# Kernel tuning notes

Hardware: AMD Instinct MI355X
Metric: run time of the kernel (lower is better)

## Reference

```python
import jax, jax.numpy as jnp
import numpy as np

N_NODES = 100000   # number of graph nodes
N_EDGES = 1000000  # number of edges
D_IN = 64          # input feature dim
D_OUT = 64         # output feature dim
N_RELS = 16        # number of relation types


def setup_inputs() -> dict:
    key = jax.random.key(0)
    k1, k2, k3, k4, k5 = jax.random.split(key, 5)
    feat = jax.random.normal(k1, (N_NODES, D_IN), dtype=jnp.float32)
    weight = jax.random.normal(k2, (N_RELS, D_IN, D_OUT), dtype=jnp.float32) * 0.05
    src = jax.random.randint(k3, (N_EDGES,), 0, N_NODES)
    dst = jax.random.randint(k4, (N_EDGES,), 0, N_NODES)
    etypes = jax.random.randint(k5, (N_EDGES,), 0, N_RELS)
    return {"feat": feat, "weight": weight, "src": src, "dst": dst, "etypes": etypes}


def reference(feat, weight, src, dst, etypes):
    # gather source-node features per edge: h = edges.src['h']
    h = feat[src]                                # [E, d_in]
    n_rels = weight.shape[0]
    e, d_out = h.shape[0], weight.shape[2]

    # gather_mm(h, weight, idx_b=etypes): m_e = h_e @ weight[etypes_e]
    # grouped-GEMM realized as R masked dense GEMMs (R is small, fixed);
    # avoids materializing the [E, d_in, d_out] gathered weight tensor.
    def step(m, rw):
        r, w_r = rw
        mask = jnp.where(etypes == r, 1.0, 0.0).astype(h.dtype)  # [E]
        m = m + mask[:, None] * (h @ w_r)                        # [E, d_out]
        return m, None

    m0 = jnp.zeros((e, d_out), dtype=h.dtype)
    m, _ = jax.lax.scan(step, m0, (jnp.arange(n_rels), weight))

    # update_all(..., fn.sum('m', 'h')): scatter-sum messages to dst nodes
    out = jax.ops.segment_sum(m, dst, num_segments=feat.shape[0])  # [N, d_out]
    return out
```

## Files before the change

kernel.cpp:

```cpp
#include <hip/hip_runtime.h>
#include <hip/hip_bf16.h>
#include <stdint.h>

#define NNODES 100000
#define NEDGES 1000000
#define NRELS 16
#define EPB 2048
#define NB ((NEDGES + EPB - 1) / EPB)
#define PADCAP (NEDGES + NRELS * 64)
#define MAXTILES (PADCAP / 64)
#define NDN NNODES
#define BKT 256
#define NBKT ((NDN + BKT - 1) / BKT)

#define FEAT_BLKS 6250
#define W_BLKS 256
#define SETUP_BLKS (FEAT_BLKS + W_BLKS + NB)
#define SCANS_BLKS (1 + (NBKT + 15) / 16)

#define OFF_FEATB    0ull
#define OFF_WT       12800000ull
#define OFF_HIST16   12931072ull
#define OFF_BBASE16  12963840ull
#define OFF_PVE      12996608ull
#define OFF_HIST391  12996864ull
#define OFF_BBASE391 13764864ull
#define OFF_BSTART   14532864ull
#define OFF_DNSTART  14534912ull
#define OFF_KEYP     14935552ull
#define OFF_INV      18935552ull
#define OFF_SRCS     22939648ull
#define OFF_MSGE     26943744ull
#define WS_NEED 155074816ull

using short8  = __attribute__((ext_vector_type(8))) short;
using floatx4 = __attribute__((ext_vector_type(4))) float;
using uintx4  = __attribute__((ext_vector_type(4))) unsigned int;

__device__ __forceinline__ unsigned short f2bf(float f) {
    union { float f; uint32_t u; } v; v.f = f;
    uint32_t u = v.u;
    return (unsigned short)((u + 0x7FFFu + ((u >> 16) & 1u)) >> 16);
}
__device__ __forceinline__ float bf2f(uint32_t u16) {
    union { uint32_t u; float f; } v; v.u = u16 << 16;
    return v.f;
}
__device__ __forceinline__ uint32_t pk2(float a, float b) {
    __hip_bfloat162 h = __float22bfloat162_rn(make_float2(a, b));
    union { __hip_bfloat162 h; uint32_t u; } v; v.h = h;
    return v.u;
}

__global__ void k_setup(const float* __restrict__ feat, const float* __restrict__ W,
                        const int* __restrict__ et, const int* __restrict__ dst,
                        unsigned short* __restrict__ featB, unsigned short* __restrict__ Wt,
                        int* __restrict__ hist16, int* __restrict__ hist391) {
    __shared__ int cnt16[16];
    __shared__ int cnt391[NBKT];
    const int b = blockIdx.x;
    if (b < FEAT_BLKS) {
        int i = (b * 256 + threadIdx.x) * 4;
        const float4 f = *(const float4*)(feat + i);
        ushort4 o;
        o.x = f2bf(f.x); o.y = f2bf(f.y); o.z = f2bf(f.z); o.w = f2bf(f.w);
        *(ushort4*)(featB + i) = o;
    } else if (b < FEAT_BLKS + W_BLKS) {
        int t = (b - FEAT_BLKS) * 256 + threadIdx.x;
        int r = t >> 12, n = (t >> 6) & 63, k = t & 63;
        Wt[t] = f2bf(W[(r << 12) + (k << 6) + n]);
    } else {
        const int bb = b - (FEAT_BLKS + W_BLKS);
        if (threadIdx.x < 16) cnt16[threadIdx.x] = 0;
        for (int t = threadIdx.x; t < NBKT; t += 256) cnt391[t] = 0;
        __syncthreads();
        int start = bb * EPB;
        int end = min(NEDGES, start + EPB);
        for (int i = start + threadIdx.x; i < end; i += 256) {
            atomicAdd(&cnt16[et[i]], 1);
            atomicAdd(&cnt391[dst[i] >> 8], 1);
        }
        __syncthreads();
        if (threadIdx.x < 16) hist16[bb * 16 + threadIdx.x] = cnt16[threadIdx.x];
        for (int t = threadIdx.x; t < NBKT; t += 256)
            hist391[bb * NBKT + t] = cnt391[t];
    }
}

__global__ void __launch_bounds__(1024)
k_scans(const int* __restrict__ hist16, int* __restrict__ bbase16,
        int* __restrict__ Pve,
        const int* __restrict__ hist391, int* __restrict__ bbase391,
        int* __restrict__ bstart) {
    int w = threadIdx.x >> 6;
    int lane = threadIdx.x & 63;
    if (blockIdx.x == 0) {
        __shared__ int s_cnt[16];
        __shared__ int s_P[17];
        int carry = 0;
        for (int c = 0; c < NB; c += 64) {
            int idx = c + lane;
            int v = (idx < NB) ? hist16[idx * 16 + w] : 0;
            int x = v;
            #pragma unroll
            for (int off = 1; off < 64; off <<= 1) {
                int y = __shfl_up(x, off);
                if (lane >= off) x += y;
            }
            if (idx < NB) bbase16[idx * 16 + w] = carry + x - v;
            carry += __shfl(x, 63);
        }
        if (lane == 0) s_cnt[w] = carry;
        __syncthreads();
        if (threadIdx.x == 0) {
            int p = 0;
            for (int r = 0; r < 16; ++r) {
                s_P[r] = p;
                Pve[r] = p;
                Pve[17 + r] = p + s_cnt[r];
                p += (s_cnt[r] + 63) & ~63;
            }
            s_P[16] = p;
            Pve[16] = p;
        }
        __syncthreads();
        int pw = s_P[w];
        for (int idx = lane; idx < NB; idx += 64)
            bbase16[idx * 16 + w] += pw;
    } else {
        int b = (blockIdx.x - 1) * 16 + w;
        if (b >= NBKT) return;
        int carry = 0;
        for (int c = 0; c < NB; c += 64) {
            int idx = c + lane;
            int v = (idx < NB) ? hist391[idx * NBKT + b] : 0;
            int x = v;
            #pragma unroll
            for (int off = 1; off < 64; off <<= 1) {
                int y = __shfl_up(x, off);
                if (lane >= off) x += y;
            }
            if (idx < NB) bbase391[idx * NBKT + b] = carry + x - v;
            carry += __shfl(x, 63);
        }
        if (lane == 0) bstart[b] = carry;
    }
}

__global__ void k_bscanB(int* __restrict__ bstart) {
    __shared__ int wtot[8];
    int t = threadIdx.x;
    int v = (t < NBKT) ? bstart[t] : 0;
    int lane = t & 63, w = t >> 6;
    int x = v;
    #pragma unroll
    for (int off = 1; off < 64; off <<= 1) {
        int y = __shfl_up(x, off);
        if (lane >= off) x += y;
    }
    if (lane == 63) wtot[w] = x;
    __syncthreads();
    int woff = 0;
    for (int i = 0; i < w; ++i) woff += wtot[i];
    if (t < NBKT) bstart[t] = woff + x - v;
    if (t == 511) {
        int total = 0;
        for (int i = 0; i < 8; ++i) total += wtot[i];
        bstart[NBKT] = total;
    }
}

__global__ void k_scatter(const int* __restrict__ et, const int* __restrict__ src,
                          const int* __restrict__ dst, const int* __restrict__ bbase16,
                          const int* __restrict__ bbase391, const int* __restrict__ bstart,
                          int* __restrict__ srcS, int* __restrict__ keyP) {
    __shared__ int base16[16];
    __shared__ int base391[NBKT];
    if (threadIdx.x < 16) base16[threadIdx.x] = bbase16[blockIdx.x * 16 + threadIdx.x];
    for (int t = threadIdx.x; t < NBKT; t += 256)
        base391[t] = bbase391[blockIdx.x * NBKT + t] + bstart[t];
    __syncthreads();
    int start = blockIdx.x * EPB;
    int end = min(NEDGES, start + EPB);
    for (int i = start + threadIdx.x; i < end; i += 256) {
        int r = et[i];
        int pos = atomicAdd(&base16[r], 1);
        srcS[pos] = src[i];
        int d = dst[i];
        int bp = atomicAdd(&base391[d >> 8], 1);
        keyP[bp] = (pos << 8) | (d & 255);
    }
}

__global__ void __launch_bounds__(256)
k_bsort(const int* __restrict__ keyP, const int* __restrict__ bstart,
        int* __restrict__ inv, int* __restrict__ dnstart) {
    __shared__ int cnt[256];
    __shared__ int nodebase[256];
    __shared__ int wtot[4];
    const int b = blockIdx.x;
    const int start = bstart[b], end = bstart[b + 1];
    const int t = threadIdx.x;
    cnt[t] = 0;
    __syncthreads();
    for (int e = start + t; e < end; e += 256)
        atomicAdd(&cnt[keyP[e] & 255], 1);
    __syncthreads();
    int v = cnt[t];
    int lane = t & 63, w = t >> 6;
    int x = v;
    #pragma unroll
    for (int off = 1; off < 64; off <<= 1) {
        int y = __shfl_up(x, off);
        if (lane >= off) x += y;
    }
    if (lane == 63) wtot[w] = x;
    __syncthreads();
    int woff = 0;
    for (int i = 0; i < w; ++i) woff += wtot[i];
    nodebase[t] = woff + x - v;
    cnt[t] = 0;
    __syncthreads();
    dnstart[b * 256 + t] = start + nodebase[t];
    if (b == NBKT - 1 && t == 255) dnstart[NBKT * 256] = end;
    for (int e = start + t; e < end; e += 256) {
        int k = keyP[e];
        int node = k & 255;
        int rk = atomicAdd(&cnt[node], 1);
        inv[k >> 8] = start + nodebase[node] + rk;
    }
}

__global__ void __launch_bounds__(256)
k_computeA(const unsigned short* __restrict__ featB,
           const unsigned short* __restrict__ Wt,
           const int* __restrict__ srcS, const int* __restrict__ Pve,
           const int* __restrict__ inv,
           unsigned short* __restrict__ msgE) {
    __shared__ float lds[4][16 * 68];
    const int w = threadIdx.x >> 6;
    const int t = blockIdx.x * 4 + w;
    const int base = t * 64;
    const int total = Pve[16];
    if (base >= total) return;
    int r = 0;
    while (base >= Pve[r + 1]) ++r;
    const int validEnd = Pve[17 + r];
    const int lane = threadIdx.x & 63;
    const int quad = lane >> 4;
    const int l16 = lane & 15;
    const int rr = lane >> 2, seg = lane & 3;

    int s[4];
    #pragma unroll
    for (int tm = 0; tm < 4; ++tm) {
        int row = base + tm * 16 + l16;
        s[tm] = (row < validEnd) ? srcS[row] : 0;
    }
    int dpos[4]; bool vld[4];
    #pragma unroll
    for (int tm = 0; tm < 4; ++tm) {
        int g = base + tm * 16 + rr;
        vld[tm] = (g < validEnd);
        dpos[tm] = vld[tm] ? inv[g] : 0;
    }
    const unsigned short* wr = Wt + (r << 12);
    short8 bfr[4][2];
    #pragma unroll
    for (int tn = 0; tn < 4; ++tn)
        #pragma unroll
        for (int ks = 0; ks < 2; ++ks)
            bfr[tn][ks] = *(const short8*)(wr + ((tn * 16 + l16) << 6) + ks * 32 + quad * 8);
    short8 a[4][2];
    #pragma unroll
    for (int tm = 0; tm < 4; ++tm) {
        const unsigned short* fp = featB + ((size_t)s[tm] << 6) + quad * 8;
        a[tm][0] = *(const short8*)(fp);
        a[tm][1] = *(const short8*)(fp + 32);
    }
    #pragma unroll
    for (int tm = 0; tm < 4; ++tm) {
        #pragma unroll
        for (int tn = 0; tn < 4; ++tn) {
            floatx4 c = {0.f, 0.f, 0.f, 0.f};
            c = __builtin_amdgcn_mfma_f32_16x16x32_bf16(a[tm][0], bfr[tn][0], c, 0, 0, 0);
            c = __builtin_amdgcn_mfma_f32_16x16x32_bf16(a[tm][1], bfr[tn][1], c, 0, 0, 0);
            #pragma unroll
            for (int j = 0; j < 4; ++j)
                lds[w][(quad * 4 + j) * 68 + tn * 16 + l16] = c[j];
        }
        if (vld[tm]) {
            const float* lp = &lds[w][rr * 68 + seg * 16];
            uintx4 o0, o1;
            o0.x = pk2(lp[0],  lp[1]);  o0.y = pk2(lp[2],  lp[3]);
            o0.z = pk2(lp[4],  lp[5]);  o0.w = pk2(lp[6],  lp[7]);
            o1.x = pk2(lp[8],  lp[9]);  o1.y = pk2(lp[10], lp[11]);
            o1.z = pk2(lp[12], lp[13]); o1.w = pk2(lp[14], lp[15]);
            uintx4* op = (uintx4*)(msgE + (size_t)dpos[tm] * 64 + seg * 16);
            op[0] = o0;
            op[1] = o1;
        }
    }
}

__global__ void __launch_bounds__(256)
k_reduce(const unsigned short* __restrict__ msgE,
         const int* __restrict__ dnstart, float* __restrict__ out) {
    int n = blockIdx.x * 4 + (threadIdx.x >> 6);
    if (n >= NDN) return;
    int lane = threadIdx.x & 63;
    int start = dnstart[n];
    int end = dnstart[n + 1];
    int c8 = (lane & 7) * 8;
    float a0 = 0.f, a1 = 0.f, a2 = 0.f, a3 = 0.f;
    float a4 = 0.f, a5 = 0.f, a6 = 0.f, a7 = 0.f;
    int row = start + (lane >> 3);
    for (; row + 8 < end; row += 16) {
        uintx4 v0 = *(const uintx4*)(msgE + (size_t)row * 64 + c8);
        uintx4 v1 = *(const uintx4*)(msgE + (size_t)(row + 8) * 64 + c8);
        a0 += bf2f(v0.x & 0xffffu); a1 += bf2f(v0.x >> 16);
        a2 += bf2f(v0.y & 0xffffu); a3 += bf2f(v0.y >> 16);
        a4 += bf2f(v0.z & 0xffffu); a5 += bf2f(v0.z >> 16);
        a6 += bf2f(v0.w & 0xffffu); a7 += bf2f(v0.w >> 16);
        a0 += bf2f(v1.x & 0xffffu); a1 += bf2f(v1.x >> 16);
        a2 += bf2f(v1.y & 0xffffu); a3 += bf2f(v1.y >> 16);
        a4 += bf2f(v1.z & 0xffffu); a5 += bf2f(v1.z >> 16);
        a6 += bf2f(v1.w & 0xffffu); a7 += bf2f(v1.w >> 16);
    }
    if (row < end) {
        uintx4 v = *(const uintx4*)(msgE + (size_t)row * 64 + c8);
        a0 += bf2f(v.x & 0xffffu); a1 += bf2f(v.x >> 16);
        a2 += bf2f(v.y & 0xffffu); a3 += bf2f(v.y >> 16);
        a4 += bf2f(v.z & 0xffffu); a5 += bf2f(v.z >> 16);
        a6 += bf2f(v.w & 0xffffu); a7 += bf2f(v.w >> 16);
    }
    #pragma unroll
    for (int m = 8; m <= 32; m <<= 1) {
        a0 += __shfl_xor(a0, m); a1 += __shfl_xor(a1, m);
        a2 += __shfl_xor(a2, m); a3 += __shfl_xor(a3, m);
        a4 += __shfl_xor(a4, m); a5 += __shfl_xor(a5, m);
        a6 += __shfl_xor(a6, m); a7 += __shfl_xor(a7, m);
    }
    if (lane < 8) {
        float* op = out + (size_t)n * 64 + lane * 8;
        *(float4*)(op)     = make_float4(a0, a1, a2, a3);
        *(float4*)(op + 4) = make_float4(a4, a5, a6, a7);
    }
}

__global__ void __launch_bounds__(256)
k_fb(const float* __restrict__ feat, const float* __restrict__ W,
     const int* __restrict__ src, const int* __restrict__ dst,
     const int* __restrict__ et, float* __restrict__ out) {
    int e = blockIdx.x * 4 + (threadIdx.x >> 6);
    if (e >= NEDGES) return;
    int c = threadIdx.x & 63;
    int s = src[e], d = dst[e], r = et[e];
    const float* fr = feat + (size_t)s * 64;
    const float* wr = W + ((size_t)r << 12);
    float acc = 0.f;
    for (int k = 0; k < 64; ++k) acc += fr[k] * wr[k * 64 + c];
    atomicAdd(out + (size_t)d * 64 + c, acc);
}

extern "C" void kernel_launch(void* const* d_in, const int* in_sizes, int n_in,
                              void* d_out, int out_size, void* d_ws, size_t ws_size,
                              hipStream_t stream) {
    const float* feat = (const float*)d_in[0];
    const float* W    = (const float*)d_in[1];
    const int* src    = (const int*)d_in[2];
    const int* dst    = (const int*)d_in[3];
    const int* et     = (const int*)d_in[4];
    float* out = (float*)d_out;
    char* ws = (char*)d_ws;

    unsigned short* featB = (unsigned short*)(ws + OFF_FEATB);
    unsigned short* Wt    = (unsigned short*)(ws + OFF_WT);
    int* hist16   = (int*)(ws + OFF_HIST16);
    int* bbase16  = (int*)(ws + OFF_BBASE16);
    int* Pve      = (int*)(ws + OFF_PVE);
    int* hist391  = (int*)(ws + OFF_HIST391);
    int* bbase391 = (int*)(ws + OFF_BBASE391);
    int* bstart   = (int*)(ws + OFF_BSTART);
    int* dnstart  = (int*)(ws + OFF_DNSTART);
    int* keyP     = (int*)(ws + OFF_KEYP);
    int* inv      = (int*)(ws + OFF_INV);
    int* srcS     = (int*)(ws + OFF_SRCS);
    unsigned short* msgE = (unsigned short*)(ws + OFF_MSGE);

    if (ws_size >= WS_NEED) {
        k_setup<<<SETUP_BLKS, 256, 0, stream>>>(feat, W, et, dst, featB, Wt,
                                                hist16, hist391);
        k_scans<<<SCANS_BLKS, 1024, 0, stream>>>(hist16, bbase16, Pve, hist391,
                                                 bbase391, bstart);
        k_bscanB<<<1, 512, 0, stream>>>(bstart);
        k_scatter<<<NB, 256, 0, stream>>>(et, src, dst, bbase16, bbase391, bstart,
                                          srcS, keyP);
        k_bsort<<<NBKT, 256, 0, stream>>>(keyP, bstart, inv, dnstart);
        k_computeA<<<(MAXTILES + 3) / 4, 256, 0, stream>>>(featB, Wt, srcS, Pve,
                                                           inv, msgE);
        k_reduce<<<(NDN + 3) / 4, 256, 0, stream>>>(msgE, dnstart, out);
    } else {
        hipMemsetAsync(d_out, 0, (size_t)out_size * sizeof(float), stream);
        k_fb<<<(NEDGES + 3) / 4, 256, 0, stream>>>(feat, W, src, dst, et, out);
    }
}
```

Before: 226.5 us.

## Sort edges by relation and source-node block to improve gather locality

The edge sort key changes from relation type alone to relation type plus a 512-node source block. Edges within each relation are then ordered by source locality, so feature gathers in the GEMM kernel hit cache more often. The cost is a much larger per-block histogram (3136 bins), a serial column scan, and a new finalize kernel. The message write-back in the compute kernel is also reshaped so each lane stores 8 bf16 values instead of 16.

```diff
diff --git a/kernel.cpp b/kernel.cpp
--- a/kernel.cpp
+++ b/kernel.cpp
@@ -10,28 +10,33 @@
 #define PADCAP (NEDGES + NRELS * 64)
 #define MAXTILES (PADCAP / 64)
 #define NDN NNODES
-#define BKT 256
-#define NBKT ((NDN + BKT - 1) / BKT)
+#define NBKT ((NDN + 255) / 256)
+#define NSB  ((NNODES + 511) / 512)
+#define NSBKT (NRELS * NSB)
 
 #define FEAT_BLKS 6250
 #define W_BLKS 256
 #define SETUP_BLKS (FEAT_BLKS + W_BLKS + NB)
-#define SCANS_BLKS (1 + (NBKT + 15) / 16)
-
-#define OFF_FEATB    0ull
-#define OFF_WT       12800000ull
-#define OFF_HIST16   12931072ull
-#define OFF_BBASE16  12963840ull
-#define OFF_PVE      12996608ull
-#define OFF_HIST391  12996864ull
-#define OFF_BBASE391 13764864ull
-#define OFF_BSTART   14532864ull
-#define OFF_DNSTART  14534912ull
-#define OFF_KEYP     14935552ull
-#define OFF_INV      18935552ull
-#define OFF_SRCS     22939648ull
-#define OFF_MSGE     26943744ull
-#define WS_NEED 155074816ull
+#define DST_SCAN_BLKS ((NBKT + 15) / 16)
+#define SRC_SCAN_BLKS ((NSBKT + 1023) / 1024)
+#define SCANS_BLKS (DST_SCAN_BLKS + SRC_SCAN_BLKS)
+
+#define OFF_FEATB     0ull
+#define OFF_WT        12800000ull
+#define OFF_COLSUM    12931072ull
+#define OFF_BKB       12943616ull
+#define OFF_PVE       12956160ull
+#define OFF_HIST391   12956416ull
+#define OFF_BBASE391  13721344ull
+#define OFF_BSTART    14486272ull
+#define OFF_DNSTART   14488064ull
+#define OFF_KEYP      14888704ull
+#define OFF_INV       18888704ull
+#define OFF_SRCS      22892800ull
+#define OFF_MSGE      26896896ull
+#define OFF_HIST3136  26896896ull
+#define OFF_BBASE3136 33030912ull
+#define WS_NEED 155027968ull
 
 using short8  = __attribute__((ext_vector_type(8))) short;
 using floatx4 = __attribute__((ext_vector_type(4))) float;
@@ -53,10 +58,11 @@
 }
 
 __global__ void k_setup(const float* __restrict__ feat, const float* __restrict__ W,
-                        const int* __restrict__ et, const int* __restrict__ dst,
+                        const int* __restrict__ et, const int* __restrict__ src,
+                        const int* __restrict__ dst,
                         unsigned short* __restrict__ featB, unsigned short* __restrict__ Wt,
-                        int* __restrict__ hist16, int* __restrict__ hist391) {
-    __shared__ int cnt16[16];
+                        int* __restrict__ hist3136, int* __restrict__ hist391) {
+    __shared__ int cnt3136[NSBKT];
     __shared__ int cnt391[NBKT];
     const int b = blockIdx.x;
     if (b < FEAT_BLKS) {
@@ -71,64 +77,32 @@
         Wt[t] = f2bf(W[(r << 12) + (k << 6) + n]);
     } else {
         const int bb = b - (FEAT_BLKS + W_BLKS);
-        if (threadIdx.x < 16) cnt16[threadIdx.x] = 0;
+        for (int t = threadIdx.x; t < NSBKT; t += 256) cnt3136[t] = 0;
         for (int t = threadIdx.x; t < NBKT; t += 256) cnt391[t] = 0;
         __syncthreads();
         int start = bb * EPB;
         int end = min(NEDGES, start + EPB);
         for (int i = start + threadIdx.x; i < end; i += 256) {
-            atomicAdd(&cnt16[et[i]], 1);
+            atomicAdd(&cnt3136[et[i] * NSB + (src[i] >> 9)], 1);
             atomicAdd(&cnt391[dst[i] >> 8], 1);
         }
         __syncthreads();
-        if (threadIdx.x < 16) hist16[bb * 16 + threadIdx.x] = cnt16[threadIdx.x];
+        for (int t = threadIdx.x; t < NSBKT; t += 256)
+            hist3136[bb * NSBKT + t] = cnt3136[t];
         for (int t = threadIdx.x; t < NBKT; t += 256)
             hist391[bb * NBKT + t] = cnt391[t];
     }
 }
 
 __global__ void __launch_bounds__(1024)
-k_scans(const int* __restrict__ hist16, int* __restrict__ bbase16,
-        int* __restrict__ Pve,
-        const int* __restrict__ hist391, int* __restrict__ bbase391,
-        int* __restrict__ bstart) {
-    int w = threadIdx.x >> 6;
-    int lane = threadIdx.x & 63;
-    if (blockIdx.x == 0) {
-        __shared__ int s_cnt[16];
-        __shared__ int s_P[17];
-        int carry = 0;
-        for (int c = 0; c < NB; c += 64) {
-            int idx = c + lane;
-            int v = (idx < NB) ? hist16[idx * 16 + w] : 0;
-            int x = v;
-            #pragma unroll
-            for (int off = 1; off < 64; off <<= 1) {
-                int y = __shfl_up(x, off);
-                if (lane >= off) x += y;
-            }
-            if (idx < NB) bbase16[idx * 16 + w] = carry + x - v;
-            carry += __shfl(x, 63);
-        }
-        if (lane == 0) s_cnt[w] = carry;
-        __syncthreads();
-        if (threadIdx.x == 0) {
-            int p = 0;
-            for (int r = 0; r < 16; ++r) {
-                s_P[r] = p;
-                Pve[r] = p;
-                Pve[17 + r] = p + s_cnt[r];
-                p += (s_cnt[r] + 63) & ~63;
-            }
-            s_P[16] = p;
-            Pve[16] = p;
-        }
-        __syncthreads();
-        int pw = s_P[w];
-        for (int idx = lane; idx < NB; idx += 64)
-            bbase16[idx * 16 + w] += pw;
-    } else {
-        int b = (blockIdx.x - 1) * 16 + w;
+k_scans(const int* __restrict__ hist391, int* __restrict__ bbase391,
+        int* __restrict__ bstart,
+        const int* __restrict__ hist3136, int* __restrict__ bbase3136,
+        int* __restrict__ colsum) {
+    if (blockIdx.x < DST_SCAN_BLKS) {
+        int w = threadIdx.x >> 6;
+        int lane = threadIdx.x & 63;
+        int b = blockIdx.x * 16 + w;
         if (b >= NBKT) return;
         int carry = 0;
         for (int c = 0; c < NB; c += 64) {
@@ -144,48 +118,101 @@
             carry += __shfl(x, 63);
         }
         if (lane == 0) bstart[b] = carry;
-    }
-}
-
-__global__ void k_bscanB(int* __restrict__ bstart) {
-    __shared__ int wtot[8];
-    int t = threadIdx.x;
-    int v = (t < NBKT) ? bstart[t] : 0;
-    int lane = t & 63, w = t >> 6;
-    int x = v;
-    #pragma unroll
-    for (int off = 1; off < 64; off <<= 1) {
-        int y = __shfl_up(x, off);
-        if (lane >= off) x += y;
-    }
-    if (lane == 63) wtot[w] = x;
-    __syncthreads();
-    int woff = 0;
-    for (int i = 0; i < w; ++i) woff += wtot[i];
-    if (t < NBKT) bstart[t] = woff + x - v;
-    if (t == 511) {
-        int total = 0;
-        for (int i = 0; i < 8; ++i) total += wtot[i];
-        bstart[NBKT] = total;
+    } else {
+        int col = (blockIdx.x - DST_SCAN_BLKS) * 1024 + threadIdx.x;
+        if (col >= NSBKT) return;
+        int carry = 0;
+        #pragma unroll 4
+        for (int i = 0; i < NB; ++i) {
+            int v = hist3136[i * NSBKT + col];
+            bbase3136[i * NSBKT + col] = carry;
+            carry += v;
+        }
+        colsum[col] = carry;
+    }
+}
+
+__global__ void __launch_bounds__(1024)
+k_finalize(int* __restrict__ bstart, const int* __restrict__ colsum,
+           int* __restrict__ bucketbase, int* __restrict__ Pve) {
+    if (blockIdx.x == 0) {
+        __shared__ int wtot[16];
+        int t = threadIdx.x;
+        int v = (t < NBKT) ? bstart[t] : 0;
+        int lane = t & 63, w = t >> 6;
+        int x = v;
+        #pragma unroll
+        for (int off = 1; off < 64; off <<= 1) {
+            int y = __shfl_up(x, off);
+            if (lane >= off) x += y;
+        }
+        if (lane == 63) wtot[w] = x;
+        __syncthreads();
+        int woff = 0;
+        for (int i = 0; i < w; ++i) woff += wtot[i];
+        if (t < NBKT) bstart[t] = woff + x - v;
+        if (t == 1023) {
+            int total = 0;
+            for (int i = 0; i < 16; ++i) total += wtot[i];
+            bstart[NBKT] = total;
+        }
+    } else {
+        __shared__ int sbb[NRELS][NSB];
+        __shared__ int s_cnt[16];
+        __shared__ int s_P[16];
+        int lane = threadIdx.x & 63, r = threadIdx.x >> 6;
+        int carry = 0;
+        for (int c = 0; c < NSB; c += 64) {
+            int idx = c + lane;
+            int v = (idx < NSB) ? colsum[r * NSB + idx] : 0;
+            int x = v;
+            #pragma unroll
+            for (int off = 1; off < 64; off <<= 1) {
+                int y = __shfl_up(x, off);
+                if (lane >= off) x += y;
+            }
+            if (idx < NSB) sbb[r][idx] = carry + x - v;
+            carry += __shfl(x, 63);
+        }
+        if (lane == 0) s_cnt[r] = carry;
+        __syncthreads();
+        if (threadIdx.x == 0) {
+            int p = 0;
+            for (int q = 0; q < 16; ++q) {
+                s_P[q] = p;
+                Pve[q] = p;
+                Pve[17 + q] = p + s_cnt[q];
+                p += (s_cnt[q] + 63) & ~63;
+            }
+            Pve[16] = p;
+        }
+        __syncthreads();
+        int pr = s_P[r];
+        for (int idx = lane; idx < NSB; idx += 64)
+            bucketbase[r * NSB + idx] = sbb[r][idx] + pr;
     }
 }
 
 __global__ void k_scatter(const int* __restrict__ et, const int* __restrict__ src,
-                          const int* __restrict__ dst, const int* __restrict__ bbase16,
+                          const int* __restrict__ dst,
+                          const int* __restrict__ bbase3136,
+                          const int* __restrict__ bucketbase,
                           const int* __restrict__ bbase391, const int* __restrict__ bstart,
                           int* __restrict__ srcS, int* __restrict__ keyP) {
-    __shared__ int base16[16];
+    __shared__ int base3136[NSBKT];
     __shared__ int base391[NBKT];
-    if (threadIdx.x < 16) base16[threadIdx.x] = bbase16[blockIdx.x * 16 + threadIdx.x];
+    for (int t = threadIdx.x; t < NSBKT; t += 256)
+        base3136[t] = bbase3136[blockIdx.x * NSBKT + t] + bucketbase[t];
     for (int t = threadIdx.x; t < NBKT; t += 256)
         base391[t] = bbase391[blockIdx.x * NBKT + t] + bstart[t];
     __syncthreads();
     int start = blockIdx.x * EPB;
     int end = min(NEDGES, start + EPB);
     for (int i = start + threadIdx.x; i < end; i += 256) {
-        int r = et[i];
-        int pos = atomicAdd(&base16[r], 1);
-        srcS[pos] = src[i];
+        int s = src[i];
+        int k = et[i] * NSB + (s >> 9);
+        int pos = atomicAdd(&base3136[k], 1);
+        srcS[pos] = s;
         int d = dst[i];
         int bp = atomicAdd(&base391[d >> 8], 1);
         keyP[bp] = (pos << 8) | (d & 255);
@@ -249,7 +276,7 @@
     const int lane = threadIdx.x & 63;
     const int quad = lane >> 4;
     const int l16 = lane & 15;
-    const int rr = lane >> 2, seg = lane & 3;
+    const int j8 = lane >> 3, s8 = lane & 7;
 
     int s[4];
     #pragma unroll
@@ -257,13 +284,15 @@
         int row = base + tm * 16 + l16;
         s[tm] = (row < validEnd) ? srcS[row] : 0;
     }
-    int dpos[4]; bool vld[4];
-    #pragma unroll
-    for (int tm = 0; tm < 4; ++tm) {
-        int g = base + tm * 16 + rr;
-        vld[tm] = (g < validEnd);
-        dpos[tm] = vld[tm] ? inv[g] : 0;
-    }
+    int dpos[4][2]; bool vld[4][2];
+    #pragma unroll
+    for (int tm = 0; tm < 4; ++tm)
+        #pragma unroll
+        for (int g = 0; g < 2; ++g) {
+            int gg = base + tm * 16 + g * 8 + j8;
+            vld[tm][g] = (gg < validEnd);
+            dpos[tm][g] = vld[tm][g] ? inv[gg] : 0;
+        }
     const unsigned short* wr = Wt + (r << 12);
     short8 bfr[4][2];
     #pragma unroll
@@ -289,16 +318,15 @@
             for (int j = 0; j < 4; ++j)
                 lds[w][(quad * 4 + j) * 68 + tn * 16 + l16] = c[j];
         }
-        if (vld[tm]) {
-            const float* lp = &lds[w][rr * 68 + seg * 16];
-            uintx4 o0, o1;
-            o0.x = pk2(lp[0],  lp[1]);  o0.y = pk2(lp[2],  lp[3]);
-            o0.z = pk2(lp[4],  lp[5]);  o0.w = pk2(lp[6],  lp[7]);
-            o1.x = pk2(lp[8],  lp[9]);  o1.y = pk2(lp[10], lp[11]);
-            o1.z = pk2(lp[12], lp[13]); o1.w = pk2(lp[14], lp[15]);
-            uintx4* op = (uintx4*)(msgE + (size_t)dpos[tm] * 64 + seg * 16);
-            op[0] = o0;
-            op[1] = o1;
+        #pragma unroll
+        for (int g = 0; g < 2; ++g) {
+            if (vld[tm][g]) {
+                const float* lp = &lds[w][(g * 8 + j8) * 68 + s8 * 8];
+                uintx4 o;
+                o.x = pk2(lp[0], lp[1]); o.y = pk2(lp[2], lp[3]);
+                o.z = pk2(lp[4], lp[5]); o.w = pk2(lp[6], lp[7]);
+                *(uintx4*)(msgE + (size_t)dpos[tm][g] * 64 + s8 * 8) = o;
+            }
         }
     }
 }
@@ -376,26 +404,28 @@
 
     unsigned short* featB = (unsigned short*)(ws + OFF_FEATB);
     unsigned short* Wt    = (unsigned short*)(ws + OFF_WT);
-    int* hist16   = (int*)(ws + OFF_HIST16);
-    int* bbase16  = (int*)(ws + OFF_BBASE16);
-    int* Pve      = (int*)(ws + OFF_PVE);
-    int* hist391  = (int*)(ws + OFF_HIST391);
-    int* bbase391 = (int*)(ws + OFF_BBASE391);
-    int* bstart   = (int*)(ws + OFF_BSTART);
-    int* dnstart  = (int*)(ws + OFF_DNSTART);
-    int* keyP     = (int*)(ws + OFF_KEYP);
-    int* inv      = (int*)(ws + OFF_INV);
-    int* srcS     = (int*)(ws + OFF_SRCS);
+    int* colsum     = (int*)(ws + OFF_COLSUM);
+    int* bucketbase = (int*)(ws + OFF_BKB);
+    int* Pve        = (int*)(ws + OFF_PVE);
+    int* hist391    = (int*)(ws + OFF_HIST391);
+    int* bbase391   = (int*)(ws + OFF_BBASE391);
+    int* bstart     = (int*)(ws + OFF_BSTART);
+    int* dnstart    = (int*)(ws + OFF_DNSTART);
+    int* keyP       = (int*)(ws + OFF_KEYP);
+    int* inv        = (int*)(ws + OFF_INV);
+    int* srcS       = (int*)(ws + OFF_SRCS);
+    int* hist3136   = (int*)(ws + OFF_HIST3136);
+    int* bbase3136  = (int*)(ws + OFF_BBASE3136);
     unsigned short* msgE = (unsigned short*)(ws + OFF_MSGE);
 
     if (ws_size >= WS_NEED) {
-        k_setup<<<SETUP_BLKS, 256, 0, stream>>>(feat, W, et, dst, featB, Wt,
-                                                hist16, hist391);
-        k_scans<<<SCANS_BLKS, 1024, 0, stream>>>(hist16, bbase16, Pve, hist391,
-                                                 bbase391, bstart);
-        k_bscanB<<<1, 512, 0, stream>>>(bstart);
-        k_scatter<<<NB, 256, 0, stream>>>(et, src, dst, bbase16, bbase391, bstart,
-                                          srcS, keyP);
+        k_setup<<<SETUP_BLKS, 256, 0, stream>>>(feat, W, et, src, dst, featB, Wt,
+                                                hist3136, hist391);
+        k_scans<<<SCANS_BLKS, 1024, 0, stream>>>(hist391, bbase391, bstart,
+                                                 hist3136, bbase3136, colsum);
+        k_finalize<<<2, 1024, 0, stream>>>(bstart, colsum, bucketbase, Pve);
+        k_scatter<<<NB, 256, 0, stream>>>(et, src, dst, bbase3136, bucketbase,
+                                          bbase391, bstart, srcS, keyP);
         k_bsort<<<NBKT, 256, 0, stream>>>(keyP, bstart, inv, dnstart);
         k_computeA<<<(MAXTILES + 3) / 4, 256, 0, stream>>>(featB, Wt, srcS, Pve,
                                                            inv, msgE);
```

Measured after the change: 305.0 us. 1.35x slower.
